# Kernel optimization log

Measured on AMD Instinct MI355X. Metric: run time of the kernel, lower is better.

## Reference

```python
import jax, jax.numpy as jnp
import numpy as np

NUM_NODES, MEM_DIM, MSG_DIM, TIME_DIM = 65536, 128, 128, 128
POS_DIM = MEM_DIM  # PositionMessage reshape forces pos_embedding_dim == memory_dim
IN_MEM = MSG_DIM + 2 * MEM_DIM + TIME_DIM  # IdentityMessage width = 512
IN_POS = POS_DIM + 2 * MEM_DIM + TIME_DIM  # PositionMessage width = 512


def setup_inputs() -> dict:
    key = jax.random.key(0)
    ks = jax.random.split(key, 24)
    s = jnp.float32(0.05)
    f = lambda k, sh: jax.random.normal(k, sh, jnp.float32)
    return dict(
        n_id=jnp.arange(NUM_NODES, dtype=jnp.int32),
        memory=f(ks[0], (NUM_NODES, MEM_DIM)),
        pos_mem=f(ks[1], (NUM_NODES, MEM_DIM)),
        pos_emb=f(ks[2], (NUM_NODES, POS_DIM)),
        raw_msg_s=f(ks[3], (NUM_NODES, MSG_DIM)),
        raw_msg_d=f(ks[4], (NUM_NODES, MSG_DIM)),
        other_s=jax.random.randint(ks[5], (NUM_NODES,), 0, NUM_NODES, jnp.int32),
        other_d=jax.random.randint(ks[6], (NUM_NODES,), 0, NUM_NODES, jnp.int32),
        t_s=jax.random.randint(ks[7], (NUM_NODES,), 1000, 2000, jnp.int32),
        t_d=jax.random.randint(ks[8], (NUM_NODES,), 1000, 2000, jnp.int32),
        last_update=jax.random.randint(ks[9], (NUM_NODES,), 0, 1000, jnp.int32),
        w_time_mem=f(ks[10], (TIME_DIM,)) * s, b_time_mem=f(ks[11], (TIME_DIM,)) * s,
        w_time_pos=f(ks[12], (TIME_DIM,)) * s, b_time_pos=f(ks[13], (TIME_DIM,)) * s,
        Wih_mem=f(ks[14], (3 * MEM_DIM, IN_MEM)) * s, Whh_mem=f(ks[15], (3 * MEM_DIM, MEM_DIM)) * s,
        bih_mem=f(ks[16], (3 * MEM_DIM,)) * s, bhh_mem=f(ks[17], (3 * MEM_DIM,)) * s,
        Wih_pos=f(ks[18], (3 * MEM_DIM, IN_POS)) * s, Whh_pos=f(ks[19], (3 * MEM_DIM, MEM_DIM)) * s,
        bih_pos=f(ks[20], (3 * MEM_DIM,)) * s, bhh_pos=f(ks[21], (3 * MEM_DIM,)) * s,
    )


def _time_enc(t_rel, w, b):
    # PyG TimeEncoder: cos(Linear(1, time_dim)(t_rel))
    return jnp.cos(t_rel[:, None] * w[None, :] + b[None, :])


def _gru(x, h, Wih, Whh, bih, bhh):
    # torch.nn.GRUCell math
    gi = x @ Wih.T + bih
    gh = h @ Whh.T + bhh
    ir, iz, inn = jnp.split(gi, 3, axis=-1)
    hr, hz, hn = jnp.split(gh, 3, axis=-1)
    r = jax.nn.sigmoid(ir + hr)
    z = jax.nn.sigmoid(iz + hz)
    n = jnp.tanh(inn + r * hn)
    return (1.0 - z) * n + z * h


def _tgn_memory(mem, n_id, other_s, other_d, feat_s, feat_d, t_s, t_d,
                last_update, w_t, b_t, Wih, Whh, bih, bhh):
    # Gather per-node state; each node owns one src-store and one dst-store message.
    h = mem[n_id]                                        # [N, D]
    lu = last_update[n_id].astype(jnp.float32)
    te_s = _time_enc(t_s.astype(jnp.float32) - lu, w_t, b_t)
    te_d = _time_enc(t_d.astype(jnp.float32) - lu, w_t, b_t)
    msg_s = jnp.concatenate([h, mem[other_s], feat_s, te_s], axis=-1)  # [N, IN]
    msg_d = jnp.concatenate([h, mem[other_d], feat_d, te_d], axis=-1)
    # LastAggregator: keep the most recent message per node (scatter_max on t)
    pick_s = (t_s >= t_d)[:, None]
    aggr = jnp.where(pick_s, msg_s, msg_d)
    z = _gru(aggr, h, Wih, Whh, bih, bhh)
    new_lu = jnp.maximum(t_s, t_d)
    return z, new_lu


def reference(n_id, memory, pos_mem, pos_emb, raw_msg_s, raw_msg_d,
              other_s, other_d, t_s, t_d, last_update,
              w_time_mem, b_time_mem, w_time_pos, b_time_pos,
              Wih_mem, Whh_mem, bih_mem, bhh_mem,
              Wih_pos, Whh_pos, bih_pos, bhh_pos):
    z, last_up = _tgn_memory(memory, n_id, other_s, other_d, raw_msg_s, raw_msg_d,
                             t_s, t_d, last_update,
                             w_time_mem, b_time_mem, Wih_mem, Whh_mem, bih_mem, bhh_mem)
    # pos raw message is the event's src node id -> embedding lookup
    pos_z, _ = _tgn_memory(pos_mem, n_id, other_s, other_d,
                           pos_emb[n_id], pos_emb[other_d],
                           t_s, t_d, last_update,
                           w_time_pos, b_time_pos, Wih_pos, Whh_pos, bih_pos, bhh_pos)
    return z, pos_z, last_up
```

## Files before the change

### kernel.cpp

```cpp
#include <hip/hip_runtime.h>
#include <hip/hip_bf16.h>
#include <math.h>

#define NODES   65536
#define DD      128
#define BM      64
#define NSUB    24
#define WTILE_STRIDE (NSUB * 64 * 8)
#define WG_STRIDE    (20 * WTILE_STRIDE)

typedef __bf16 bf16x8 __attribute__((ext_vector_type(8)));
typedef float  f32x4  __attribute__((ext_vector_type(4)));

static __device__ __forceinline__ float fastcos(float x) {
    float r = x * 0.15915494309189535f;
    r = r - floorf(r);
    return __builtin_amdgcn_cosf(r);
}
static __device__ __forceinline__ float fsigmoid(float x) {
    return 1.0f / (1.0f + __expf(-x));
}
static __device__ __forceinline__ float ftanh(float x) {
    float ax = fabsf(x);
    float t  = __expf(-2.0f * ax);
    float th = 1.0f - 2.0f * t / (1.0f + t);
    return copysignf(th, x);
}
static __device__ __forceinline__ uint2 cvtpk4(float4 v) {
    uint2 r;
    asm("v_cvt_pk_bf16_f32 %0, %1, %2" : "=v"(r.x) : "v"(v.x), "v"(v.y));
    asm("v_cvt_pk_bf16_f32 %0, %1, %2" : "=v"(r.y) : "v"(v.z), "v"(v.w));
    return r;
}
static __device__ __forceinline__ unsigned short f2bf(float f) {
    union { float f; unsigned u; } v; v.f = f;
    return (unsigned short)((v.u + 0x8000u) >> 16);
}

__global__ void prep_w_kernel(const float* __restrict__ Wih0, const float* __restrict__ Whh0,
                              const float* __restrict__ Wih1, const float* __restrict__ Whh1,
                              unsigned short* __restrict__ Wws) {
    int gid = blockIdx.x * 256 + threadIdx.x;
    if (gid >= 2 * WG_STRIDE) return;
    int g   = gid / WG_STRIDE;
    int r   = gid - g * WG_STRIDE;
    int kt  = r / WTILE_STRIDE;
    int r2  = r - kt * WTILE_STRIDE;
    int t   = r2 >> 9;
    int l8  = r2 & 511;
    int lane = l8 >> 3, j = l8 & 7;
    int cl  = lane & 15, q = lane >> 4;
    int n   = t * 16 + cl;
    const float* Wih = g ? Wih1 : Wih0;
    const float* Whh = g ? Whh1 : Whh0;
    float v;
    if (kt < 16) v = Wih[n * 512 + kt * 32 + q * 8 + j];
    else         v = Whh[n * 128 + (kt - 16) * 32 + q * 8 + j];
    Wws[gid] = f2bf(v);
}


#define KTILE(st, kt, sn)                                                      \
    do {                                                                       \
        bf16x8 a[4];                                                           \
        _Pragma("unroll")                                                      \
        for (int j = 0; j < 4; ++j)                                            \
            a[j] = *(const bf16x8*)(Xb + (j * 16 + cl) * 1024 +                \
                                    (((st) * 64 + q * 16) ^ swz));             \
        const unsigned short* wk = wbase + (size_t)(kt) * WTILE_STRIDE;        \
        bf16x8 bR = *(const bf16x8*)(wk + tR * 512);                           \
        bf16x8 bZ = *(const bf16x8*)(wk + tZ * 512);                           \
        bf16x8 bN = *(const bf16x8*)(wk + tN * 512);                           \
        _Pragma("unroll")                                                      \
        for (int j = 0; j < 4; ++j) {                                          \
            acc[j * 4 + 0]  = __builtin_amdgcn_mfma_f32_16x16x32_bf16(a[j], bR, acc[j * 4 + 0], 0, 0, 0);  \
            acc[j * 4 + 1]  = __builtin_amdgcn_mfma_f32_16x16x32_bf16(a[j], bZ, acc[j * 4 + 1], 0, 0, 0);  \
            acc[j * 4 + sn] = __builtin_amdgcn_mfma_f32_16x16x32_bf16(a[j], bN, acc[j * 4 + sn], 0, 0, 0); \
        }                                                                      \
    } while (0)

__global__ __launch_bounds__(512, 4) void tgn_fused_kernel(
    const int*   __restrict__ n_id,
    const float* __restrict__ memory_,
    const float* __restrict__ pos_mem,
    const float* __restrict__ pos_emb,
    const float* __restrict__ raw_s,
    const float* __restrict__ raw_d,
    const int*   __restrict__ other_s,
    const int*   __restrict__ other_d,
    const int*   __restrict__ t_s,
    const int*   __restrict__ t_d,
    const int*   __restrict__ last_update,
    const float* __restrict__ w_time_mem, const float* __restrict__ b_time_mem,
    const float* __restrict__ w_time_pos, const float* __restrict__ b_time_pos,
    const float* __restrict__ bih_mem, const float* __restrict__ bhh_mem,
    const float* __restrict__ bih_pos, const float* __restrict__ bhh_pos,
    const unsigned short* __restrict__ Wws,
    float* __restrict__ out)
{
    __shared__ __align__(16) unsigned short X[BM * 512];
    __shared__ int   snid[BM];
    __shared__ int   soth[BM];
    __shared__ float sdt[BM];
    __shared__ int   sfeat[BM];

    const int g   = blockIdx.y;
    const int nb  = blockIdx.x;
    const int tid = threadIdx.x;
    const int lane = tid & 63;
    const int wv   = tid >> 6;

    const float* mem_g = g ? pos_mem    : memory_;
    const float* wt    = g ? w_time_pos : w_time_mem;
    const float* bt    = g ? b_time_pos : b_time_mem;
    const float* bih   = g ? bih_pos    : bih_mem;
    const float* bhh   = g ? bhh_pos    : bhh_mem;

    if (tid < BM) {
        int gi   = nb * BM + tid;
        int id   = n_id[gi];
        int ts   = t_s[gi];
        int td   = t_d[gi];
        bool pick = (ts >= td);
        int oth  = pick ? other_s[gi] : other_d[gi];
        int lu   = last_update[id];
        float dt = (float)(pick ? ts : td) - (float)lu;
        int code;
        if (g) code = pick ? id : other_d[gi];
        else   code = pick ? gi : ~gi;
        snid[tid]  = id;
        soth[tid]  = oth;
        sdt[tid]   = dt;
        sfeat[tid] = code;
        if (g == 0) {
            out[2 * (size_t)NODES * DD + gi] = (float)max(ts, td);
        }
    }
    __syncthreads();

    const int lc    = lane & 31;
    const int rh    = lane >> 5;
    const int srow0 = wv * 8;

    float4 of[4];
    #pragma unroll
    for (int c = 0; c < 4; ++c) {
        int row = srow0 + 2 * c + rh;
        of[c] = *(const float4*)(mem_g + (size_t)soth[row] * DD + lc * 4);
    }
    __builtin_amdgcn_sched_barrier(0);

    #pragma unroll
    for (int c = 0; c < 4; ++c) {
        int row = srow0 + 2 * c + rh;
        float4 v = *(const float4*)(mem_g + (size_t)snid[row] * DD + lc * 4);
        *(uint2*)((char*)X + row * 1024 + ((lc * 8) ^ ((row & 7) << 4))) = cvtpk4(v);
    }
    #pragma unroll
    for (int c = 0; c < 4; ++c) {
        int row = srow0 + 2 * c + rh;
        float dt = sdt[row];
        float4 wv4 = *(const float4*)(wt + lc * 4);
        float4 bv4 = *(const float4*)(bt + lc * 4);
        float4 tv;
        tv.x = fastcos(dt * wv4.x + bv4.x);
        tv.y = fastcos(dt * wv4.y + bv4.y);
        tv.z = fastcos(dt * wv4.z + bv4.z);
        tv.w = fastcos(dt * wv4.w + bv4.w);
        *(uint2*)((char*)X + row * 1024 + ((768 + lc * 8) ^ ((row & 7) << 4))) = cvtpk4(tv);
    }
    __syncthreads();

    f32x4 acc[16];
    #pragma unroll
    for (int i = 0; i < 16; ++i) acc[i] = (f32x4){0.f, 0.f, 0.f, 0.f};

    const int q  = lane >> 4;
    const int cl = lane & 15;
    const int swz = (cl & 7) << 4;
    const unsigned short* wbase = Wws + (size_t)g * WG_STRIDE + lane * 8;
    const int tR = wv, tZ = 8 + wv, tN = 16 + wv;
    const char* Xb = (const char*)X;

    __builtin_amdgcn_s_setprio(1);
    KTILE(0, 0, 2);  KTILE(0, 16, 3);
    KTILE(1, 1, 2);  KTILE(1, 17, 3);
    KTILE(2, 2, 2);  KTILE(2, 18, 3);
    KTILE(3, 3, 2);  KTILE(3, 19, 3);
    __builtin_amdgcn_s_setprio(0);

    #pragma unroll
    for (int c = 0; c < 4; ++c) {
        int row = srow0 + 2 * c + rh;
        *(uint2*)((char*)X + row * 1024 + ((256 + lc * 8) ^ ((row & 7) << 4))) = cvtpk4(of[c]);
    }

    float4 ff[4];
    #pragma unroll
    for (int c = 0; c < 4; ++c) {
        int row = srow0 + 2 * c + rh;
        const float* src;
        if (g) {
            src = pos_emb + (size_t)sfeat[row] * DD;
        } else {
            int code = sfeat[row];
            src = code >= 0 ? raw_s + (size_t)code * DD
                            : raw_d + (size_t)(~code) * DD;
        }
        ff[c] = *(const float4*)(src + lc * 4);
    }
    __builtin_amdgcn_sched_barrier(0);

    __builtin_amdgcn_s_setprio(1);
    KTILE(12, 12, 2); KTILE(13, 13, 2); KTILE(14, 14, 2); KTILE(15, 15, 2);
    __builtin_amdgcn_s_setprio(0);

    #pragma unroll
    for (int c = 0; c < 4; ++c) {
        int row = srow0 + 2 * c + rh;
        *(uint2*)((char*)X + row * 1024 + ((512 + lc * 8) ^ ((row & 7) << 4))) = cvtpk4(ff[c]);
    }
    __syncthreads();

    __builtin_amdgcn_s_setprio(1);
    KTILE(4, 4, 2);   KTILE(5, 5, 2);   KTILE(6, 6, 2);   KTILE(7, 7, 2);
    KTILE(8, 8, 2);   KTILE(9, 9, 2);   KTILE(10, 10, 2); KTILE(11, 11, 2);
    __builtin_amdgcn_s_setprio(0);

    float* outz = out + (size_t)g * NODES * DD;
    const int d = wv * 16 + cl;
    float br  = bih[d]       + bhh[d];
    float bz  = bih[128 + d] + bhh[128 + d];
    float bni = bih[256 + d];
    float bnh = bhh[256 + d];
    #pragma unroll
    for (int j = 0; j < 4; ++j) {
        #pragma unroll
        for (int r = 0; r < 4; ++r) {
            int il = j * 16 + q * 4 + r;
            float rs  = acc[j * 4 + 0][r] + br;
            float zs  = acc[j * 4 + 1][r] + bz;
            float in_ = acc[j * 4 + 2][r] + bni;
            float hn_ = acc[j * 4 + 3][r] + bnh;
            float rg = fsigmoid(rs);
            float zg = fsigmoid(zs);
            float nv = ftanh(in_ + rg * hn_);
            float h  = mem_g[(size_t)snid[il] * DD + d];
            outz[(size_t)(nb * BM + il) * DD + d] = (1.0f - zg) * nv + zg * h;
        }
    }
}

extern "C" void kernel_launch(void* const* d_in, const int* in_sizes, int n_in,
                              void* d_out, int out_size, void* d_ws, size_t ws_size,
                              hipStream_t stream) {
    const int*   n_id        = (const int*)  d_in[0];
    const float* memory_     = (const float*)d_in[1];
    const float* pos_mem     = (const float*)d_in[2];
    const float* pos_emb     = (const float*)d_in[3];
    const float* raw_s       = (const float*)d_in[4];
    const float* raw_d       = (const float*)d_in[5];
    const int*   other_s     = (const int*)  d_in[6];
    const int*   other_d     = (const int*)  d_in[7];
    const int*   t_s         = (const int*)  d_in[8];
    const int*   t_d         = (const int*)  d_in[9];
    const int*   last_update = (const int*)  d_in[10];
    const float* w_time_mem  = (const float*)d_in[11];
    const float* b_time_mem  = (const float*)d_in[12];
    const float* w_time_pos  = (const float*)d_in[13];
    const float* b_time_pos  = (const float*)d_in[14];
    const float* Wih_mem     = (const float*)d_in[15];
    const float* Whh_mem     = (const float*)d_in[16];
    const float* bih_mem     = (const float*)d_in[17];
    const float* bhh_mem     = (const float*)d_in[18];
    const float* Wih_pos     = (const float*)d_in[19];
    const float* Whh_pos     = (const float*)d_in[20];
    const float* bih_pos     = (const float*)d_in[21];
    const float* bhh_pos     = (const float*)d_in[22];

    unsigned short* Wws = (unsigned short*)d_ws;
    float* out = (float*)d_out;

    prep_w_kernel<<<(2 * WG_STRIDE + 255) / 256, 256, 0, stream>>>(
        Wih_mem, Whh_mem, Wih_pos, Whh_pos, Wws);

    dim3 grid(NODES / BM, 2);
    tgn_fused_kernel<<<grid, 512, 0, stream>>>(
        n_id, memory_, pos_mem, pos_emb, raw_s, raw_d,
        other_s, other_d, t_s, t_d, last_update,
        w_time_mem, b_time_mem, w_time_pos, b_time_pos,
        bih_mem, bhh_mem, bih_pos, bhh_pos,
        Wws, out);
}
```

Before: 309.9 us.

## Gather all inputs before a single barrier, then run the full MFMA chain

Removes the staged overlap between gather loads and partial MFMA tiles. All four input segments (h, other memory, features, time encoding) are now loaded and written to LDS before one barrier, followed by all K tiles in sequence, with the h-tile and Whh work merged into one macro. It also replaces the packed bf16 conversion asm with a scalar round-to-nearest conversion and hoists the time-weight loads out of the loop. This simplifies the schedule but gives up hiding gather latency behind MFMA work and adds conversion instructions.

```diff
diff --git a/kernel.cpp b/kernel.cpp
--- a/kernel.cpp
+++ b/kernel.cpp
@@ -12,6 +12,15 @@
 typedef __bf16 bf16x8 __attribute__((ext_vector_type(8)));
 typedef float  f32x4  __attribute__((ext_vector_type(4)));
 
+static __device__ __forceinline__ unsigned short f2bf(float f) {
+    union { float f; unsigned u; } v; v.f = f;
+    return (unsigned short)((v.u + 0x8000u) >> 16);
+}
+static __device__ __forceinline__ ushort4 pack4(float4 v) {
+    ushort4 p;
+    p.x = f2bf(v.x); p.y = f2bf(v.y); p.z = f2bf(v.z); p.w = f2bf(v.w);
+    return p;
+}
 static __device__ __forceinline__ float fastcos(float x) {
     float r = x * 0.15915494309189535f;
     r = r - floorf(r);
@@ -25,16 +34,6 @@
     float t  = __expf(-2.0f * ax);
     float th = 1.0f - 2.0f * t / (1.0f + t);
     return copysignf(th, x);
-}
-static __device__ __forceinline__ uint2 cvtpk4(float4 v) {
-    uint2 r;
-    asm("v_cvt_pk_bf16_f32 %0, %1, %2" : "=v"(r.x) : "v"(v.x), "v"(v.y));
-    asm("v_cvt_pk_bf16_f32 %0, %1, %2" : "=v"(r.y) : "v"(v.z), "v"(v.w));
-    return r;
-}
-static __device__ __forceinline__ unsigned short f2bf(float f) {
-    union { float f; unsigned u; } v; v.f = f;
-    return (unsigned short)((v.u + 0x8000u) >> 16);
 }
 
 __global__ void prep_w_kernel(const float* __restrict__ Wih0, const float* __restrict__ Whh0,
@@ -60,22 +59,48 @@
 }
 
 
-#define KTILE(st, kt, sn)                                                      \
+#define KTILE(st)                                                              \
     do {                                                                       \
         bf16x8 a[4];                                                           \
         _Pragma("unroll")                                                      \
         for (int j = 0; j < 4; ++j)                                            \
             a[j] = *(const bf16x8*)(Xb + (j * 16 + cl) * 1024 +                \
                                     (((st) * 64 + q * 16) ^ swz));             \
-        const unsigned short* wk = wbase + (size_t)(kt) * WTILE_STRIDE;        \
+        const unsigned short* wk = wbase + (size_t)(st) * WTILE_STRIDE;        \
         bf16x8 bR = *(const bf16x8*)(wk + tR * 512);                           \
         bf16x8 bZ = *(const bf16x8*)(wk + tZ * 512);                           \
         bf16x8 bN = *(const bf16x8*)(wk + tN * 512);                           \
         _Pragma("unroll")                                                      \
         for (int j = 0; j < 4; ++j) {                                          \
-            acc[j * 4 + 0]  = __builtin_amdgcn_mfma_f32_16x16x32_bf16(a[j], bR, acc[j * 4 + 0], 0, 0, 0);  \
-            acc[j * 4 + 1]  = __builtin_amdgcn_mfma_f32_16x16x32_bf16(a[j], bZ, acc[j * 4 + 1], 0, 0, 0);  \
-            acc[j * 4 + sn] = __builtin_amdgcn_mfma_f32_16x16x32_bf16(a[j], bN, acc[j * 4 + sn], 0, 0, 0); \
+            acc[j * 4 + 0] = __builtin_amdgcn_mfma_f32_16x16x32_bf16(a[j], bR, acc[j * 4 + 0], 0, 0, 0); \
+            acc[j * 4 + 1] = __builtin_amdgcn_mfma_f32_16x16x32_bf16(a[j], bZ, acc[j * 4 + 1], 0, 0, 0); \
+            acc[j * 4 + 2] = __builtin_amdgcn_mfma_f32_16x16x32_bf16(a[j], bN, acc[j * 4 + 2], 0, 0, 0); \
+        }                                                                      \
+    } while (0)
+
+#define KTILE2(st)                                                             \
+    do {                                                                       \
+        bf16x8 a[4];                                                           \
+        _Pragma("unroll")                                                      \
+        for (int j = 0; j < 4; ++j)                                            \
+            a[j] = *(const bf16x8*)(Xb + (j * 16 + cl) * 1024 +                \
+                                    (((st) * 64 + q * 16) ^ swz));             \
+        const unsigned short* wk = wbase + (size_t)(st) * WTILE_STRIDE;        \
+        const unsigned short* wh = wbase + (size_t)(16 + (st)) * WTILE_STRIDE; \
+        bf16x8 bR = *(const bf16x8*)(wk + tR * 512);                           \
+        bf16x8 bZ = *(const bf16x8*)(wk + tZ * 512);                           \
+        bf16x8 bN = *(const bf16x8*)(wk + tN * 512);                           \
+        bf16x8 cR = *(const bf16x8*)(wh + tR * 512);                           \
+        bf16x8 cZ = *(const bf16x8*)(wh + tZ * 512);                           \
+        bf16x8 cN = *(const bf16x8*)(wh + tN * 512);                           \
+        _Pragma("unroll")                                                      \
+        for (int j = 0; j < 4; ++j) {                                          \
+            acc[j * 4 + 0] = __builtin_amdgcn_mfma_f32_16x16x32_bf16(a[j], bR, acc[j * 4 + 0], 0, 0, 0); \
+            acc[j * 4 + 1] = __builtin_amdgcn_mfma_f32_16x16x32_bf16(a[j], bZ, acc[j * 4 + 1], 0, 0, 0); \
+            acc[j * 4 + 2] = __builtin_amdgcn_mfma_f32_16x16x32_bf16(a[j], bN, acc[j * 4 + 2], 0, 0, 0); \
+            acc[j * 4 + 0] = __builtin_amdgcn_mfma_f32_16x16x32_bf16(a[j], cR, acc[j * 4 + 0], 0, 0, 0); \
+            acc[j * 4 + 1] = __builtin_amdgcn_mfma_f32_16x16x32_bf16(a[j], cZ, acc[j * 4 + 1], 0, 0, 0); \
+            acc[j * 4 + 3] = __builtin_amdgcn_mfma_f32_16x16x32_bf16(a[j], cN, acc[j * 4 + 3], 0, 0, 0); \
         }                                                                      \
     } while (0)
 
@@ -142,6 +167,16 @@
     const int rh    = lane >> 5;
     const int srow0 = wv * 8;
 
+    float4 wv4 = *(const float4*)(wt + lc * 4);
+    float4 bv4 = *(const float4*)(bt + lc * 4);
+    __builtin_amdgcn_sched_barrier(0);
+    float4 hv[4];
+    #pragma unroll
+    for (int c = 0; c < 4; ++c) {
+        int row = srow0 + 2 * c + rh;
+        hv[c] = *(const float4*)(mem_g + (size_t)snid[row] * DD + lc * 4);
+    }
+    __builtin_amdgcn_sched_barrier(0);
     float4 of[4];
     #pragma unroll
     for (int c = 0; c < 4; ++c) {
@@ -153,48 +188,19 @@
     #pragma unroll
     for (int c = 0; c < 4; ++c) {
         int row = srow0 + 2 * c + rh;
-        float4 v = *(const float4*)(mem_g + (size_t)snid[row] * DD + lc * 4);
-        *(uint2*)((char*)X + row * 1024 + ((lc * 8) ^ ((row & 7) << 4))) = cvtpk4(v);
-    }
-    #pragma unroll
-    for (int c = 0; c < 4; ++c) {
-        int row = srow0 + 2 * c + rh;
         float dt = sdt[row];
-        float4 wv4 = *(const float4*)(wt + lc * 4);
-        float4 bv4 = *(const float4*)(bt + lc * 4);
         float4 tv;
         tv.x = fastcos(dt * wv4.x + bv4.x);
         tv.y = fastcos(dt * wv4.y + bv4.y);
         tv.z = fastcos(dt * wv4.z + bv4.z);
         tv.w = fastcos(dt * wv4.w + bv4.w);
-        *(uint2*)((char*)X + row * 1024 + ((768 + lc * 8) ^ ((row & 7) << 4))) = cvtpk4(tv);
-    }
-    __syncthreads();
-
-    f32x4 acc[16];
-    #pragma unroll
-    for (int i = 0; i < 16; ++i) acc[i] = (f32x4){0.f, 0.f, 0.f, 0.f};
-
-    const int q  = lane >> 4;
-    const int cl = lane & 15;
-    const int swz = (cl & 7) << 4;
-    const unsigned short* wbase = Wws + (size_t)g * WG_STRIDE + lane * 8;
-    const int tR = wv, tZ = 8 + wv, tN = 16 + wv;
-    const char* Xb = (const char*)X;
-
-    __builtin_amdgcn_s_setprio(1);
-    KTILE(0, 0, 2);  KTILE(0, 16, 3);
-    KTILE(1, 1, 2);  KTILE(1, 17, 3);
-    KTILE(2, 2, 2);  KTILE(2, 18, 3);
-    KTILE(3, 3, 2);  KTILE(3, 19, 3);
-    __builtin_amdgcn_s_setprio(0);
-
-    #pragma unroll
-    for (int c = 0; c < 4; ++c) {
-        int row = srow0 + 2 * c + rh;
-        *(uint2*)((char*)X + row * 1024 + ((256 + lc * 8) ^ ((row & 7) << 4))) = cvtpk4(of[c]);
-    }
-
+        *(ushort4*)((char*)X + row * 1024 + ((768 + lc * 8) ^ ((row & 7) << 4))) = pack4(tv);
+    }
+    #pragma unroll
+    for (int c = 0; c < 4; ++c) {
+        int row = srow0 + 2 * c + rh;
+        *(ushort4*)((char*)X + row * 1024 + ((lc * 8) ^ ((row & 7) << 4))) = pack4(hv[c]);
+    }
     float4 ff[4];
     #pragma unroll
     for (int c = 0; c < 4; ++c) {
@@ -210,21 +216,34 @@
         ff[c] = *(const float4*)(src + lc * 4);
     }
     __builtin_amdgcn_sched_barrier(0);
+    #pragma unroll
+    for (int c = 0; c < 4; ++c) {
+        int row = srow0 + 2 * c + rh;
+        *(ushort4*)((char*)X + row * 1024 + ((256 + lc * 8) ^ ((row & 7) << 4))) = pack4(of[c]);
+    }
+    #pragma unroll
+    for (int c = 0; c < 4; ++c) {
+        int row = srow0 + 2 * c + rh;
+        *(ushort4*)((char*)X + row * 1024 + ((512 + lc * 8) ^ ((row & 7) << 4))) = pack4(ff[c]);
+    }
+    __syncthreads();
+
+    f32x4 acc[16];
+    #pragma unroll
+    for (int i = 0; i < 16; ++i) acc[i] = (f32x4){0.f, 0.f, 0.f, 0.f};
+
+    const int q  = lane >> 4;
+    const int cl = lane & 15;
+    const int swz = (cl & 7) << 4;
+    const unsigned short* wbase = Wws + (size_t)g * WG_STRIDE + lane * 8;
+    const int tR = wv, tZ = 8 + wv, tN = 16 + wv;
+    const char* Xb = (const char*)X;
 
     __builtin_amdgcn_s_setprio(1);
-    KTILE(12, 12, 2); KTILE(13, 13, 2); KTILE(14, 14, 2); KTILE(15, 15, 2);
-    __builtin_amdgcn_s_setprio(0);
-
-    #pragma unroll
-    for (int c = 0; c < 4; ++c) {
-        int row = srow0 + 2 * c + rh;
-        *(uint2*)((char*)X + row * 1024 + ((512 + lc * 8) ^ ((row & 7) << 4))) = cvtpk4(ff[c]);
-    }
-    __syncthreads();
-
-    __builtin_amdgcn_s_setprio(1);
-    KTILE(4, 4, 2);   KTILE(5, 5, 2);   KTILE(6, 6, 2);   KTILE(7, 7, 2);
-    KTILE(8, 8, 2);   KTILE(9, 9, 2);   KTILE(10, 10, 2); KTILE(11, 11, 2);
+    KTILE2(0); KTILE2(1); KTILE2(2); KTILE2(3);
+    KTILE(4);  KTILE(5);  KTILE(6);  KTILE(7);
+    KTILE(8);  KTILE(9);  KTILE(10); KTILE(11);
+    KTILE(12); KTILE(13); KTILE(14); KTILE(15);
     __builtin_amdgcn_s_setprio(0);
 
     float* outz = out + (size_t)g * NODES * DD;
```

Result: faster. 285.3 us (-7.9%).
